# Performance work log

Hardware: AMD Instinct MI355X
Metric: run time of the kernel (lower is better)

Reference implementation:

```python
import jax, jax.numpy as jnp
import numpy as np
from jax import lax

# Module constants (from init_kwargs)
K = 1.0            # conductivity
H = 1.0 / 1023.0   # grid spacing
VALUE = 0.0        # Dirichlet boundary value
STENCIL = np.array([[0.0, 0.25, 0.0],
                    [0.25, 0.0, 0.25],
                    [0.0, 0.25, 0.0]], dtype=np.float32)


def setup_inputs() -> dict:
    key = jax.random.key(0)
    k1, k2 = jax.random.split(key)
    B, C, Hn, Wn = 16, 1, 1024, 1024
    u = jax.random.normal(k1, (B, C, Hn, Wn), dtype=jnp.float32)
    f = jax.random.normal(k2, (B, C, Hn, Wn), dtype=jnp.float32)
    # conv weight: (out=1, in=1, 3, 3), repeated over in_channels (=1 here)
    weight = jnp.asarray(STENCIL).reshape(1, 1, 3, 3)
    return {"u": u, "f": f, "weight": weight}


def reference(u, f, weight):
    # v = detached interior of u, padded with the Dirichlet value
    v_int = lax.stop_gradient(u[..., 1:-1, 1:-1])           # [B,1,H-2,W-2]
    v = jnp.pad(v_int, ((0, 0), (0, 0), (1, 1), (1, 1)),
                mode="constant", constant_values=VALUE)      # [B,1,H,W]
    # 5-point Jacobi stencil, VALID conv -> interior shape [B,1,H-2,W-2]
    conv = lax.conv_general_dilated(
        v, weight, window_strides=(1, 1), padding="VALID",
        dimension_numbers=("NCHW", "OIHW", "NCHW"))
    cof = -(H ** 2) / (K * 4.0)
    source = lax.stop_gradient((cof * f)[..., 1:-1, 1:-1])
    # interior <- stencil(v) + source; boundary stays at Dirichlet VALUE
    out = v.at[..., 1:-1, 1:-1].set(conv + source)
    return out
```

## Files before the change

### kernel.cpp

```cpp
#include <hip/hip_runtime.h>

#define IMG_W 1024
#define IMG_H 1024

__global__ __launch_bounds__(256) void dir_rhs_kernel(
    const float* __restrict__ u,
    const float* __restrict__ f,
    const float* __restrict__ wt,
    float* __restrict__ out)
{
    const int row = blockIdx.x;
    const int b   = row >> 10;
    const int i   = row & (IMG_H - 1);
    const int tid = threadIdx.x;
    const int j0  = tid << 2;
    const size_t img = (size_t)b << 20;

    float4* out4 = (float4*)(out + img + (size_t)i * IMG_W + j0);

    if (i == 0 || i == IMG_H - 1) {
        *out4 = make_float4(0.f, 0.f, 0.f, 0.f);
        return;
    }

    const float w00 = wt[0], w01 = wt[1], w02 = wt[2];
    const float w10 = wt[3], w11 = wt[4], w12 = wt[5];
    const float w20 = wt[6], w21 = wt[7], w22 = wt[8];
    const float cof = (float)(-(1.0 / 1023.0) * (1.0 / 1023.0) / 4.0);

    const float* urow = u + img + (size_t)i * IMG_W;

    float vm[6], vc[6], vp[6];

    const bool left_edge  = (j0 == 0);
    const bool right_edge = (j0 + 4 >= IMG_W);

    {
        float4 c = *(const float4*)(urow + j0);
        vc[1] = c.x; vc[2] = c.y; vc[3] = c.z; vc[4] = c.w;
        vc[0] = left_edge  ? 0.f : urow[j0 - 1];
        vc[5] = right_edge ? 0.f : urow[j0 + 4];
        if (left_edge)  vc[1] = 0.f;
        if (right_edge) vc[4] = 0.f;
    }
    if (i == 1) {
        #pragma unroll
        for (int k = 0; k < 6; k++) vm[k] = 0.f;
    } else {
        const float* r = urow - IMG_W;
        float4 c = *(const float4*)(r + j0);
        vm[1] = c.x; vm[2] = c.y; vm[3] = c.z; vm[4] = c.w;
        vm[0] = left_edge  ? 0.f : r[j0 - 1];
        vm[5] = right_edge ? 0.f : r[j0 + 4];
        if (left_edge)  vm[1] = 0.f;
        if (right_edge) vm[4] = 0.f;
    }
    if (i == IMG_H - 2) {
        #pragma unroll
        for (int k = 0; k < 6; k++) vp[k] = 0.f;
    } else {
        const float* r = urow + IMG_W;
        float4 c = *(const float4*)(r + j0);
        vp[1] = c.x; vp[2] = c.y; vp[3] = c.z; vp[4] = c.w;
        vp[0] = left_edge  ? 0.f : r[j0 - 1];
        vp[5] = right_edge ? 0.f : r[j0 + 4];
        if (left_edge)  vp[1] = 0.f;
        if (right_edge) vp[4] = 0.f;
    }

    float4 f4 = *(const float4*)(f + img + (size_t)i * IMG_W + j0);
    float ff[4] = {f4.x, f4.y, f4.z, f4.w};

    float res[4];
    #pragma unroll
    for (int e = 0; e < 4; e++) {
        float acc = cof * ff[e];
        acc += w00 * vm[e] + w01 * vm[e + 1] + w02 * vm[e + 2];
        acc += w10 * vc[e] + w11 * vc[e + 1] + w12 * vc[e + 2];
        acc += w20 * vp[e] + w21 * vp[e + 1] + w22 * vp[e + 2];
        res[e] = acc;
    }
    if (left_edge)  res[0] = 0.f;
    if (right_edge) res[3] = 0.f;

    *out4 = make_float4(res[0], res[1], res[2], res[3]);
}

extern "C" void kernel_launch(void* const* d_in, const int* in_sizes, int n_in,
                              void* d_out, int out_size, void* d_ws, size_t ws_size,
                              hipStream_t stream) {
    const float* u  = (const float*)d_in[0];
    const float* f  = (const float*)d_in[1];
    const float* wt = (const float*)d_in[2];
    float* out = (float*)d_out;

    const int B = 16;
    dim3 grid(B * IMG_H);
    dim3 block(256);
    dir_rhs_kernel<<<grid, block, 0, stream>>>(u, f, wt, out);
}
```

Measured before the change: 168.0 us.

## Process four rows per block with register row reuse and LDS halo exchange

Each block now handles four consecutive rows. It loads the six needed input rows once into registers as float4 and shares each thread's edge values through a small shared-memory array. The goal is to remove redundant global loads of neighbouring rows and the scalar unaligned halo loads. The cost is more registers per thread, one block barrier, and a fourfold drop in block count.

```diff
diff --git a/kernel.cpp b/kernel.cpp
--- a/kernel.cpp
+++ b/kernel.cpp
@@ -2,6 +2,7 @@
 
 #define IMG_W 1024
 #define IMG_H 1024
+#define RPB   4
 
 __global__ __launch_bounds__(256) void dir_rhs_kernel(
     const float* __restrict__ u,
@@ -9,81 +10,76 @@
     const float* __restrict__ wt,
     float* __restrict__ out)
 {
-    const int row = blockIdx.x;
-    const int b   = row >> 10;
-    const int i   = row & (IMG_H - 1);
+    __shared__ float2 halo[RPB + 2][256];
+
     const int tid = threadIdx.x;
     const int j0  = tid << 2;
+    const int gb  = blockIdx.x;
+    const int b   = gb >> 8;
+    const int r0  = (gb & 255) << 2;
     const size_t img = (size_t)b << 20;
-
-    float4* out4 = (float4*)(out + img + (size_t)i * IMG_W + j0);
-
-    if (i == 0 || i == IMG_H - 1) {
-        *out4 = make_float4(0.f, 0.f, 0.f, 0.f);
-        return;
-    }
 
     const float w00 = wt[0], w01 = wt[1], w02 = wt[2];
     const float w10 = wt[3], w11 = wt[4], w12 = wt[5];
     const float w20 = wt[6], w21 = wt[7], w22 = wt[8];
     const float cof = (float)(-(1.0 / 1023.0) * (1.0 / 1023.0) / 4.0);
 
-    const float* urow = u + img + (size_t)i * IMG_W;
+    float4 stage[RPB + 2];
+    #pragma unroll
+    for (int k = 0; k < RPB + 2; k++) {
+        const int grow = r0 - 1 + k;
+        if (grow >= 1 && grow <= IMG_H - 2) {
+            stage[k] = *(const float4*)(u + img + (size_t)grow * IMG_W + j0);
+        } else {
+            stage[k] = make_float4(0.f, 0.f, 0.f, 0.f);
+        }
+    }
+    float4 fr[RPB];
+    #pragma unroll
+    for (int k = 0; k < RPB; k++) {
+        fr[k] = *(const float4*)(f + img + (size_t)(r0 + k) * IMG_W + j0);
+    }
+    #pragma unroll
+    for (int k = 0; k < RPB + 2; k++) {
+        if (tid == 0)   stage[k].x = 0.f;
+        if (tid == 255) stage[k].w = 0.f;
+        halo[k][tid] = make_float2(stage[k].x, stage[k].w);
+    }
+    __syncthreads();
 
-    float vm[6], vc[6], vp[6];
+    const int tl = (tid == 0)   ? 0   : tid - 1;
+    const int tr = (tid == 255) ? 255 : tid + 1;
 
-    const bool left_edge  = (j0 == 0);
-    const bool right_edge = (j0 + 4 >= IMG_W);
+    #pragma unroll
+    for (int k = 0; k < RPB; k++) {
+        const int grow = r0 + k;
+        float4* o4 = (float4*)(out + img + (size_t)grow * IMG_W + j0);
+        if (grow == 0 || grow == IMG_H - 1) {
+            *o4 = make_float4(0.f, 0.f, 0.f, 0.f);
+            continue;
+        }
+        float vm[6], vc[6], vp[6];
+        vm[0] = halo[k    ][tl].y;  vm[5] = halo[k    ][tr].x;
+        vc[0] = halo[k + 1][tl].y;  vc[5] = halo[k + 1][tr].x;
+        vp[0] = halo[k + 2][tl].y;  vp[5] = halo[k + 2][tr].x;
+        vm[1] = stage[k].x;     vm[2] = stage[k].y;     vm[3] = stage[k].z;     vm[4] = stage[k].w;
+        vc[1] = stage[k + 1].x; vc[2] = stage[k + 1].y; vc[3] = stage[k + 1].z; vc[4] = stage[k + 1].w;
+        vp[1] = stage[k + 2].x; vp[2] = stage[k + 2].y; vp[3] = stage[k + 2].z; vp[4] = stage[k + 2].w;
 
-    {
-        float4 c = *(const float4*)(urow + j0);
-        vc[1] = c.x; vc[2] = c.y; vc[3] = c.z; vc[4] = c.w;
-        vc[0] = left_edge  ? 0.f : urow[j0 - 1];
-        vc[5] = right_edge ? 0.f : urow[j0 + 4];
-        if (left_edge)  vc[1] = 0.f;
-        if (right_edge) vc[4] = 0.f;
+        const float ff[4] = { fr[k].x, fr[k].y, fr[k].z, fr[k].w };
+        float res[4];
+        #pragma unroll
+        for (int e = 0; e < 4; e++) {
+            float acc = cof * ff[e];
+            acc += w00 * vm[e] + w01 * vm[e + 1] + w02 * vm[e + 2];
+            acc += w10 * vc[e] + w11 * vc[e + 1] + w12 * vc[e + 2];
+            acc += w20 * vp[e] + w21 * vp[e + 1] + w22 * vp[e + 2];
+            res[e] = acc;
+        }
+        if (tid == 0)   res[0] = 0.f;
+        if (tid == 255) res[3] = 0.f;
+        *o4 = make_float4(res[0], res[1], res[2], res[3]);
     }
-    if (i == 1) {
-        #pragma unroll
-        for (int k = 0; k < 6; k++) vm[k] = 0.f;
-    } else {
-        const float* r = urow - IMG_W;
-        float4 c = *(const float4*)(r + j0);
-        vm[1] = c.x; vm[2] = c.y; vm[3] = c.z; vm[4] = c.w;
-        vm[0] = left_edge  ? 0.f : r[j0 - 1];
-        vm[5] = right_edge ? 0.f : r[j0 + 4];
-        if (left_edge)  vm[1] = 0.f;
-        if (right_edge) vm[4] = 0.f;
-    }
-    if (i == IMG_H - 2) {
-        #pragma unroll
-        for (int k = 0; k < 6; k++) vp[k] = 0.f;
-    } else {
-        const float* r = urow + IMG_W;
-        float4 c = *(const float4*)(r + j0);
-        vp[1] = c.x; vp[2] = c.y; vp[3] = c.z; vp[4] = c.w;
-        vp[0] = left_edge  ? 0.f : r[j0 - 1];
-        vp[5] = right_edge ? 0.f : r[j0 + 4];
-        if (left_edge)  vp[1] = 0.f;
-        if (right_edge) vp[4] = 0.f;
-    }
-
-    float4 f4 = *(const float4*)(f + img + (size_t)i * IMG_W + j0);
-    float ff[4] = {f4.x, f4.y, f4.z, f4.w};
-
-    float res[4];
-    #pragma unroll
-    for (int e = 0; e < 4; e++) {
-        float acc = cof * ff[e];
-        acc += w00 * vm[e] + w01 * vm[e + 1] + w02 * vm[e + 2];
-        acc += w10 * vc[e] + w11 * vc[e + 1] + w12 * vc[e + 2];
-        acc += w20 * vp[e] + w21 * vp[e + 1] + w22 * vp[e + 2];
-        res[e] = acc;
-    }
-    if (left_edge)  res[0] = 0.f;
-    if (right_edge) res[3] = 0.f;
-
-    *out4 = make_float4(res[0], res[1], res[2], res[3]);
 }
 
 extern "C" void kernel_launch(void* const* d_in, const int* in_sizes, int n_in,
@@ -95,7 +91,7 @@
     float* out = (float*)d_out;
 
     const int B = 16;
-    dim3 grid(B * IMG_H);
+    dim3 grid(B * (IMG_H / RPB));
     dim3 block(256);
     dir_rhs_kernel<<<grid, block, 0, stream>>>(u, f, wt, out);
 }
```

Result: no change. 171.0 us (+1.8%).
